# Optimization experiments

Hardware: AMD Instinct MI355X
Metric: run time of the kernel (lower is better)

Reference implementation:

```python
import jax, jax.numpy as jnp
import numpy as np

N_NODES = 100000
N_EDGES = 1600000
IN_DIM = 128
OUT_DIM = 256
EPS = 1e-12


def setup_inputs() -> dict:
    key = jax.random.key(0)
    k1, k2, k3, k4, k5 = jax.random.split(key, 5)
    x = jax.random.normal(k1, (N_NODES, IN_DIM), dtype=jnp.float32)
    edge_index = jax.random.randint(k2, (2, N_EDGES), 0, N_NODES, dtype=jnp.int64)
    edge_weight = jax.random.uniform(k3, (N_EDGES,), dtype=jnp.float32)
    # nn.Linear(in_dim*2, out_dim): weight [out, 2*in], bias [out]
    bound = 1.0 / np.sqrt(2 * IN_DIM)
    W = jax.random.uniform(k4, (OUT_DIM, 2 * IN_DIM), minval=-bound, maxval=bound, dtype=jnp.float32)
    b = jax.random.uniform(k5, (OUT_DIM,), minval=-bound, maxval=bound, dtype=jnp.float32)
    return {"x": x, "edge_index": edge_index, "edge_weight": edge_weight, "W": W, "b": b}


def reference(x, edge_index, edge_weight, W, b):
    src = edge_index[0]
    dst = edge_index[1]
    w = edge_weight.astype(x.dtype)
    # messages: [E, in_dim] = gathered dst features weighted per-edge
    messages = x[dst] * w[:, None]
    agg = jax.ops.segment_sum(messages, src, num_segments=x.shape[0])   # [N, in_dim]
    wsum = jax.ops.segment_sum(w, src, num_segments=x.shape[0])        # [N]
    neigh = agg / jnp.maximum(wsum, EPS)[:, None]
    h = jnp.concatenate([x, neigh], axis=1)                            # [N, 2*in_dim]
    h = h @ W.T + b
    return jax.nn.relu(h)  # dropout is identity in eval / p=0.0
```

## Files before the change

kernel.cpp:

```cpp
#include <hip/hip_runtime.h>
#include <hip/hip_bf16.h>

#define IN_DIM 128
#define OUT_DIM 256
#define KDIM 256
#define EPS 1e-12f
#define CB_NODES 128
#define NB_MAX 1024
#define PART_CHUNK 2048
#define CAP 2560

typedef __attribute__((ext_vector_type(8))) short short8;
typedef __attribute__((ext_vector_type(4))) float f32x4;

static __device__ __forceinline__ unsigned short f2bf(float f) {
  __hip_bfloat16 h = __float2bfloat16(f);
  return *reinterpret_cast<unsigned short*>(&h);
}
static __device__ __forceinline__ unsigned pack2bf(float a, float b) {
  return (unsigned)f2bf(a) | ((unsigned)f2bf(b) << 16);
}
static __device__ __forceinline__ float bf_lo(unsigned v) {
  return __uint_as_float((v & 0xffffu) << 16);
}
static __device__ __forceinline__ float bf_hi(unsigned v) {
  return __uint_as_float(v & 0xffff0000u);
}

__global__ __launch_bounds__(256) void cvt_x(
    const float* __restrict__ x, unsigned short* __restrict__ hb, int N) {
  const int total = N * 32;
  const int stride = gridDim.x * blockDim.x;
  for (int idx = blockIdx.x * blockDim.x + threadIdx.x; idx < total; idx += stride) {
    const int row = idx >> 5;
    const int c4 = (idx & 31) * 4;
    const float4 v = *reinterpret_cast<const float4*>(x + (size_t)row * IN_DIM + c4);
    ushort4 o;
    o.x = f2bf(v.x); o.y = f2bf(v.y); o.z = f2bf(v.z); o.w = f2bf(v.w);
    *reinterpret_cast<ushort4*>(hb + (size_t)row * KDIM + c4) = o;
  }
}

__global__ __launch_bounds__(256) void cvt_w(
    const float* __restrict__ W, unsigned short* __restrict__ Wb) {
  const int base = (blockIdx.x * blockDim.x + threadIdx.x) * 4;
  const float4 v = *reinterpret_cast<const float4*>(W + base);
  ushort4 o;
  o.x = f2bf(v.x); o.y = f2bf(v.y); o.z = f2bf(v.z); o.w = f2bf(v.w);
  *reinterpret_cast<ushort4*>(Wb + base) = o;
}

__global__ __launch_bounds__(256) void chist(
    const int* __restrict__ src, int* __restrict__ cnt, int E, int NB) {
  __shared__ int lcnt[NB_MAX];
  for (int i = threadIdx.x; i < NB; i += 256) lcnt[i] = 0;
  __syncthreads();
  const int stride = gridDim.x * blockDim.x;
  for (int e = blockIdx.x * blockDim.x + threadIdx.x; e < E; e += stride)
    atomicAdd(&lcnt[src[e] >> 7], 1);
  __syncthreads();
  for (int i = threadIdx.x; i < NB; i += 256)
    if (lcnt[i]) atomicAdd(&cnt[i], lcnt[i]);
}

__global__ void cscan(const int* __restrict__ cnt, int* __restrict__ bstart,
                      int* __restrict__ gcursor, int NB) {
  const int lane = threadIdx.x;
  int carry = 0;
  for (int base = 0; base < NB; base += 64) {
    const int i = base + lane;
    const int c = (i < NB) ? cnt[i] : 0;
    int incl = c;
    for (int d = 1; d < 64; d <<= 1) {
      int t = __shfl_up(incl, d, 64);
      if (lane >= d) incl += t;
    }
    const int excl = carry + incl - c;
    if (i < NB) { bstart[i] = excl; gcursor[i] = excl; }
    carry += __shfl(incl, 63, 64);
  }
  if (lane == 0) bstart[NB] = carry;
}

__global__ __launch_bounds__(256) void cpartition(
    const int* __restrict__ src, const int* __restrict__ dst,
    const float* __restrict__ ew,
    int* __restrict__ gcursor, int2* __restrict__ recs, int E, int NB) {
  __shared__ int pos[NB_MAX];
  const int c0 = blockIdx.x * PART_CHUNK;
  const int c1 = min(E, c0 + PART_CHUNK);
  for (int i = threadIdx.x; i < NB; i += 256) pos[i] = 0;
  __syncthreads();
  for (int i = c0 + threadIdx.x; i < c1; i += 256)
    atomicAdd(&pos[src[i] >> 7], 1);
  __syncthreads();
  for (int b = threadIdx.x; b < NB; b += 256) {
    const int c = pos[b];
    pos[b] = c ? atomicAdd(&gcursor[b], c) : 0;
  }
  __syncthreads();
  for (int i = c0 + threadIdx.x; i < c1; i += 256) {
    const int s = src[i];
    const int p = atomicAdd(&pos[s >> 7], 1);
    int2 r;
    r.x = dst[i] | ((s & 127) << 17);
    r.y = __float_as_int(ew[i]);
    recs[p] = r;
  }
}

__global__ __launch_bounds__(512, 8) void cagg_fast(
    unsigned short* __restrict__ hb,
    const int* __restrict__ bstart,
    const int2* __restrict__ recs, int N) {
  __shared__ int2 lrec[CAP];
  __shared__ int lstart[CB_NODES + 1];
  __shared__ int lcur[CB_NODES];
  const int tid = threadIdx.x;
  const int lane = tid & 63;
  const int wv = tid >> 6;
  const int blk = blockIdx.x;
  const int e0 = bstart[blk];
  const int e1 = bstart[blk + 1];
  const int m = e1 - e0;
  if (m > CAP) return;

  if (tid < CB_NODES) lcur[tid] = 0;
  __syncthreads();
  for (int i = tid; i < m; i += 512)
    atomicAdd(&lcur[recs[e0 + i].x >> 17], 1);
  __syncthreads();
  if (wv == 0) {
    int carry = 0;
#pragma unroll
    for (int rr = 0; rr < 2; ++rr) {
      const int idx = rr * 64 + lane;
      const int c = lcur[idx];
      int incl = c;
#pragma unroll
      for (int d = 1; d < 64; d <<= 1) {
        int t = __shfl_up(incl, d, 64);
        if (lane >= d) incl += t;
      }
      lstart[idx] = carry + incl - c;
      carry += __shfl(incl, 63, 64);
    }
    if (lane == 0) lstart[CB_NODES] = carry;
  }
  __syncthreads();
  if (tid < CB_NODES) lcur[tid] = lstart[tid];
  __syncthreads();
  for (int i = tid; i < m; i += 512) {
    const int2 r = recs[e0 + i];
    lrec[atomicAdd(&lcur[r.x >> 17], 1)] = r;
  }
  __syncthreads();

  for (int n = 0; n < 16; ++n) {
    const int rs = lstart[wv * 16 + n];
    const int re = lstart[wv * 16 + n + 1];
    float ax = 0.f, ay = 0.f, ws = 0.f;
    int j = rs;
    for (; j + 8 <= re; j += 8) {
      const int2 r0 = lrec[j + 0];
      const int2 r1 = lrec[j + 1];
      const int2 r2 = lrec[j + 2];
      const int2 r3 = lrec[j + 3];
      const int2 r4 = lrec[j + 4];
      const int2 r5 = lrec[j + 5];
      const int2 r6 = lrec[j + 6];
      const int2 r7 = lrec[j + 7];
      const unsigned v0 = *reinterpret_cast<const unsigned*>(hb + (size_t)(r0.x & 0x1FFFF) * KDIM + lane * 2);
      const unsigned v1 = *reinterpret_cast<const unsigned*>(hb + (size_t)(r1.x & 0x1FFFF) * KDIM + lane * 2);
      const unsigned v2 = *reinterpret_cast<const unsigned*>(hb + (size_t)(r2.x & 0x1FFFF) * KDIM + lane * 2);
      const unsigned v3 = *reinterpret_cast<const unsigned*>(hb + (size_t)(r3.x & 0x1FFFF) * KDIM + lane * 2);
      const unsigned v4 = *reinterpret_cast<const unsigned*>(hb + (size_t)(r4.x & 0x1FFFF) * KDIM + lane * 2);
      const unsigned v5 = *reinterpret_cast<const unsigned*>(hb + (size_t)(r5.x & 0x1FFFF) * KDIM + lane * 2);
      const unsigned v6 = *reinterpret_cast<const unsigned*>(hb + (size_t)(r6.x & 0x1FFFF) * KDIM + lane * 2);
      const unsigned v7 = *reinterpret_cast<const unsigned*>(hb + (size_t)(r7.x & 0x1FFFF) * KDIM + lane * 2);
      const float w0 = __int_as_float(r0.y), w1 = __int_as_float(r1.y);
      const float w2 = __int_as_float(r2.y), w3 = __int_as_float(r3.y);
      const float w4 = __int_as_float(r4.y), w5 = __int_as_float(r5.y);
      const float w6 = __int_as_float(r6.y), w7 = __int_as_float(r7.y);
      ax += bf_lo(v0) * w0 + bf_lo(v1) * w1 + bf_lo(v2) * w2 + bf_lo(v3) * w3
          + bf_lo(v4) * w4 + bf_lo(v5) * w5 + bf_lo(v6) * w6 + bf_lo(v7) * w7;
      ay += bf_hi(v0) * w0 + bf_hi(v1) * w1 + bf_hi(v2) * w2 + bf_hi(v3) * w3
          + bf_hi(v4) * w4 + bf_hi(v5) * w5 + bf_hi(v6) * w6 + bf_hi(v7) * w7;
      ws += w0 + w1 + w2 + w3 + w4 + w5 + w6 + w7;
    }
    for (; j + 2 <= re; j += 2) {
      const int2 r0 = lrec[j + 0];
      const int2 r1 = lrec[j + 1];
      const unsigned v0 = *reinterpret_cast<const unsigned*>(hb + (size_t)(r0.x & 0x1FFFF) * KDIM + lane * 2);
      const unsigned v1 = *reinterpret_cast<const unsigned*>(hb + (size_t)(r1.x & 0x1FFFF) * KDIM + lane * 2);
      const float w0 = __int_as_float(r0.y), w1 = __int_as_float(r1.y);
      ax += bf_lo(v0) * w0 + bf_lo(v1) * w1;
      ay += bf_hi(v0) * w0 + bf_hi(v1) * w1;
      ws += w0 + w1;
    }
    if (j < re) {
      const int2 r = lrec[j];
      const unsigned v = *reinterpret_cast<const unsigned*>(hb + (size_t)(r.x & 0x1FFFF) * KDIM + lane * 2);
      const float w = __int_as_float(r.y);
      ax += bf_lo(v) * w;
      ay += bf_hi(v) * w;
      ws += w;
    }
    const int node = blk * CB_NODES + wv * 16 + n;
    if (node < N) {
      const float mm = fmaxf(ws, EPS);
      *reinterpret_cast<unsigned*>(hb + (size_t)node * KDIM + IN_DIM + lane * 2) =
          pack2bf(ax / mm, ay / mm);
    }
  }
}

__global__ __launch_bounds__(512) void cagg_slow(
    unsigned short* __restrict__ hb,
    const int* __restrict__ bstart,
    const int2* __restrict__ recs, int N) {
  const int blk = blockIdx.x;
  const int e0 = bstart[blk];
  const int e1 = bstart[blk + 1];
  if (e1 - e0 <= CAP) return;

  __shared__ int2 lrec[CAP];
  __shared__ int lstart[CB_NODES + 1];
  __shared__ int lcur[CB_NODES];
  const int tid = threadIdx.x;
  const int lane = tid & 63;
  const int wv = tid >> 6;

  float ax[16], ay[16], ws[16];
#pragma unroll
  for (int n = 0; n < 16; ++n) { ax[n] = 0.f; ay[n] = 0.f; ws[n] = 0.f; }

  for (int base = e0; base < e1; base += CAP) {
    const int m = min(CAP, e1 - base);
    if (tid < CB_NODES) lcur[tid] = 0;
    __syncthreads();
    for (int i = tid; i < m; i += 512)
      atomicAdd(&lcur[recs[base + i].x >> 17], 1);
    __syncthreads();
    if (wv == 0) {
      int carry = 0;
#pragma unroll
      for (int rr = 0; rr < 2; ++rr) {
        const int idx = rr * 64 + lane;
        const int c = lcur[idx];
        int incl = c;
#pragma unroll
        for (int d = 1; d < 64; d <<= 1) {
          int t = __shfl_up(incl, d, 64);
          if (lane >= d) incl += t;
        }
        lstart[idx] = carry + incl - c;
        carry += __shfl(incl, 63, 64);
      }
      if (lane == 0) lstart[CB_NODES] = carry;
    }
    __syncthreads();
    if (tid < CB_NODES) lcur[tid] = lstart[tid];
    __syncthreads();
    for (int i = tid; i < m; i += 512) {
      const int2 r = recs[base + i];
      lrec[atomicAdd(&lcur[r.x >> 17], 1)] = r;
    }
    __syncthreads();
#pragma unroll
    for (int n = 0; n < 16; ++n) {
      const int rs = lstart[wv * 16 + n];
      const int re = lstart[wv * 16 + n + 1];
      for (int j = rs; j < re; ++j) {
        const int2 r = lrec[j];
        const unsigned v = *reinterpret_cast<const unsigned*>(
            hb + (size_t)(r.x & 0x1FFFF) * KDIM + lane * 2);
        const float w = __int_as_float(r.y);
        ax[n] += bf_lo(v) * w;
        ay[n] += bf_hi(v) * w;
        ws[n] += w;
      }
    }
    __syncthreads();
  }

#pragma unroll
  for (int n = 0; n < 16; ++n) {
    const int node = blk * CB_NODES + wv * 16 + n;
    if (node < N) {
      const float mm = fmaxf(ws[n], EPS);
      *reinterpret_cast<unsigned*>(hb + (size_t)node * KDIM + IN_DIM + lane * 2) =
          pack2bf(ax[n] / mm, ay[n] / mm);
    }
  }
}

__global__ __launch_bounds__(512, 2) void sage_gemm_mfma(
    const unsigned short* __restrict__ hb,
    const unsigned short* __restrict__ Wb,
    const float* __restrict__ bias,
    float* __restrict__ out, int N) {
  __shared__ unsigned short Wl[OUT_DIM * KDIM];
  const int tid = threadIdx.x;
  const int lane = tid & 63;
  const int wv = tid >> 6;

  char* wl = reinterpret_cast<char*>(Wl);
  const uint4* wbv = reinterpret_cast<const uint4*>(Wb);
  for (int ch = tid; ch < OUT_DIM * KDIM / 8; ch += 512) {
    const int elem = ch * 8;
    const int j = elem >> 8;
    const int col = elem & 255;
    const uint4 o = wbv[ch];
    const int byte = (j << 9) | ((col * 2) ^ ((j & 7) << 4));
    *reinterpret_cast<uint4*>(wl + byte) = o;
  }

  const int row0 = blockIdx.x * 256 + wv * 32;
  const int kc = (lane >> 4) * 8;
  const unsigned short* arow0 = hb + (size_t)(row0 + (lane & 15)) * KDIM + kc;
  const unsigned short* arow1 = arow0 + 16 * KDIM;
  short8 a0[8], a1[8];
#pragma unroll
  for (int kk = 0; kk < 8; ++kk) {
    a0[kk] = *reinterpret_cast<const short8*>(arow0 + kk * 32);
    a1[kk] = *reinterpret_cast<const short8*>(arow1 + kk * 32);
  }

  __syncthreads();

  f32x4 acc[2][16];
#pragma unroll
  for (int i = 0; i < 2; ++i)
#pragma unroll
    for (int j = 0; j < 16; ++j) acc[i][j] = (f32x4){0.f, 0.f, 0.f, 0.f};

  const int jrow = lane & 15;
  const int kb0 = kc * 2;
#pragma unroll
  for (int kk = 0; kk < 8; ++kk) {
    const int kbyte = kb0 + kk * 64;
#pragma unroll
    for (int ct = 0; ct < 16; ++ct) {
      const int j = ct * 16 + jrow;
      const short8 bf = *reinterpret_cast<const short8*>(
          wl + ((j << 9) | (kbyte ^ ((j & 7) << 4))));
      acc[0][ct] = __builtin_amdgcn_mfma_f32_16x16x32_bf16(a0[kk], bf, acc[0][ct], 0, 0, 0);
      acc[1][ct] = __builtin_amdgcn_mfma_f32_16x16x32_bf16(a1[kk], bf, acc[1][ct], 0, 0, 0);
    }
  }

  const int col = lane & 15;
  const int rquad = (lane >> 4) * 4;
#pragma unroll
  for (int ct = 0; ct < 16; ++ct) {
    const int j = ct * 16 + col;
    const float bj = bias[j];
#pragma unroll
    for (int rt = 0; rt < 2; ++rt) {
      const int rbase = row0 + rt * 16 + rquad;
      const f32x4 a = acc[rt][ct];
#pragma unroll
      for (int r = 0; r < 4; ++r) {
        const int row = rbase + r;
        if (row < N) out[(size_t)row * OUT_DIM + j] = fmaxf(a[r] + bj, 0.f);
      }
    }
  }
}

extern "C" void kernel_launch(void* const* d_in, const int* in_sizes, int n_in,
                              void* d_out, int out_size, void* d_ws, size_t ws_size,
                              hipStream_t stream) {
  const float* x  = (const float*)d_in[0];
  const int*   ei = (const int*)d_in[1];
  const float* ew = (const float*)d_in[2];
  const float* W  = (const float*)d_in[3];
  const float* b  = (const float*)d_in[4];
  float* out = (float*)d_out;

  const int N = in_sizes[0] / IN_DIM;
  const int E = in_sizes[2];
  const int* src = ei;
  const int* dst = ei + E;

  const int gemm_blocks = (N + 255) / 256;
  const int Mpad = gemm_blocks * 256;
  const int NB = (N + CB_NODES - 1) / CB_NODES;

  unsigned short* hb = (unsigned short*)d_ws;
  unsigned short* Wb = hb + (size_t)Mpad * KDIM;
  int2* recs   = (int2*)(Wb + OUT_DIM * KDIM);
  int* cnt     = (int*)(recs + E);
  int* bstart  = cnt + NB_MAX;
  int* gcursor = bstart + NB_MAX + 1;

  hipMemsetAsync(cnt, 0, NB * sizeof(int), stream);

  cvt_x<<<2048, 256, 0, stream>>>(x, hb, N);
  cvt_w<<<OUT_DIM * KDIM / 4 / 256, 256, 0, stream>>>(W, Wb);
  chist<<<512, 256, 0, stream>>>(src, cnt, E, NB);
  cscan<<<1, 64, 0, stream>>>(cnt, bstart, gcursor, NB);
  cpartition<<<(E + PART_CHUNK - 1) / PART_CHUNK, 256, 0, stream>>>(
      src, dst, ew, gcursor, recs, E, NB);
  cagg_fast<<<NB, 512, 0, stream>>>(hb, bstart, recs, N);
  cagg_slow<<<NB, 512, 0, stream>>>(hb, bstart, recs, N);
  sage_gemm_mfma<<<gemm_blocks, 512, 0, stream>>>(hb, Wb, b, out, N);
}
```

Before: 380.6 us.

## Gather neighbor rows with 16-byte loads across four edge groups per wave

The aggregation kernel now splits each wave into four 16-lane groups. Each group handles a different edge and loads 8 bf16 features per lane with uint4 loads, and the partial sums are combined with cross-lane shuffles. Previously every lane loaded 4 bytes per edge. The aim is fewer, wider memory transactions for the random gather. It adds a shuffle reduction per node and a masked tail loop. Separately, the partition kernel caches the src chunk in shared memory so src is not read from global memory twice.

```diff
diff --git a/kernel.cpp b/kernel.cpp
--- a/kernel.cpp
+++ b/kernel.cpp
@@ -87,12 +87,16 @@
     const float* __restrict__ ew,
     int* __restrict__ gcursor, int2* __restrict__ recs, int E, int NB) {
   __shared__ int pos[NB_MAX];
+  __shared__ int ssrc[PART_CHUNK];
   const int c0 = blockIdx.x * PART_CHUNK;
   const int c1 = min(E, c0 + PART_CHUNK);
   for (int i = threadIdx.x; i < NB; i += 256) pos[i] = 0;
   __syncthreads();
-  for (int i = c0 + threadIdx.x; i < c1; i += 256)
-    atomicAdd(&pos[src[i] >> 7], 1);
+  for (int i = c0 + threadIdx.x; i < c1; i += 256) {
+    const int s = src[i];
+    ssrc[i - c0] = s;
+    atomicAdd(&pos[s >> 7], 1);
+  }
   __syncthreads();
   for (int b = threadIdx.x; b < NB; b += 256) {
     const int c = pos[b];
@@ -100,7 +104,7 @@
   }
   __syncthreads();
   for (int i = c0 + threadIdx.x; i < c1; i += 256) {
-    const int s = src[i];
+    const int s = ssrc[i - c0];
     const int p = atomicAdd(&pos[s >> 7], 1);
     int2 r;
     r.x = dst[i] | ((s & 127) << 17);
@@ -156,61 +160,66 @@
   }
   __syncthreads();
 
+  const int g = lane >> 4;
+  const int fl = lane & 15;
   for (int n = 0; n < 16; ++n) {
     const int rs = lstart[wv * 16 + n];
     const int re = lstart[wv * 16 + n + 1];
-    float ax = 0.f, ay = 0.f, ws = 0.f;
-    int j = rs;
-    for (; j + 8 <= re; j += 8) {
-      const int2 r0 = lrec[j + 0];
-      const int2 r1 = lrec[j + 1];
-      const int2 r2 = lrec[j + 2];
-      const int2 r3 = lrec[j + 3];
-      const int2 r4 = lrec[j + 4];
-      const int2 r5 = lrec[j + 5];
-      const int2 r6 = lrec[j + 6];
-      const int2 r7 = lrec[j + 7];
-      const unsigned v0 = *reinterpret_cast<const unsigned*>(hb + (size_t)(r0.x & 0x1FFFF) * KDIM + lane * 2);
-      const unsigned v1 = *reinterpret_cast<const unsigned*>(hb + (size_t)(r1.x & 0x1FFFF) * KDIM + lane * 2);
-      const unsigned v2 = *reinterpret_cast<const unsigned*>(hb + (size_t)(r2.x & 0x1FFFF) * KDIM + lane * 2);
-      const unsigned v3 = *reinterpret_cast<const unsigned*>(hb + (size_t)(r3.x & 0x1FFFF) * KDIM + lane * 2);
-      const unsigned v4 = *reinterpret_cast<const unsigned*>(hb + (size_t)(r4.x & 0x1FFFF) * KDIM + lane * 2);
-      const unsigned v5 = *reinterpret_cast<const unsigned*>(hb + (size_t)(r5.x & 0x1FFFF) * KDIM + lane * 2);
-      const unsigned v6 = *reinterpret_cast<const unsigned*>(hb + (size_t)(r6.x & 0x1FFFF) * KDIM + lane * 2);
-      const unsigned v7 = *reinterpret_cast<const unsigned*>(hb + (size_t)(r7.x & 0x1FFFF) * KDIM + lane * 2);
+    float a0 = 0.f, a1 = 0.f, a2 = 0.f, a3 = 0.f;
+    float a4 = 0.f, a5 = 0.f, a6 = 0.f, a7 = 0.f, ws = 0.f;
+    int j0 = rs;
+    for (; j0 + 16 <= re; j0 += 16) {
+      const int e = j0 + g;
+      const int2 r0 = lrec[e];
+      const int2 r1 = lrec[e + 4];
+      const int2 r2 = lrec[e + 8];
+      const int2 r3 = lrec[e + 12];
+      const uint4 v0 = *reinterpret_cast<const uint4*>(hb + (size_t)(r0.x & 0x1FFFF) * KDIM + fl * 8);
+      const uint4 v1 = *reinterpret_cast<const uint4*>(hb + (size_t)(r1.x & 0x1FFFF) * KDIM + fl * 8);
+      const uint4 v2 = *reinterpret_cast<const uint4*>(hb + (size_t)(r2.x & 0x1FFFF) * KDIM + fl * 8);
+      const uint4 v3 = *reinterpret_cast<const uint4*>(hb + (size_t)(r3.x & 0x1FFFF) * KDIM + fl * 8);
       const float w0 = __int_as_float(r0.y), w1 = __int_as_float(r1.y);
       const float w2 = __int_as_float(r2.y), w3 = __int_as_float(r3.y);
-      const float w4 = __int_as_float(r4.y), w5 = __int_as_float(r5.y);
-      const float w6 = __int_as_float(r6.y), w7 = __int_as_float(r7.y);
-      ax += bf_lo(v0) * w0 + bf_lo(v1) * w1 + bf_lo(v2) * w2 + bf_lo(v3) * w3
-          + bf_lo(v4) * w4 + bf_lo(v5) * w5 + bf_lo(v6) * w6 + bf_lo(v7) * w7;
-      ay += bf_hi(v0) * w0 + bf_hi(v1) * w1 + bf_hi(v2) * w2 + bf_hi(v3) * w3
-          + bf_hi(v4) * w4 + bf_hi(v5) * w5 + bf_hi(v6) * w6 + bf_hi(v7) * w7;
-      ws += w0 + w1 + w2 + w3 + w4 + w5 + w6 + w7;
-    }
-    for (; j + 2 <= re; j += 2) {
-      const int2 r0 = lrec[j + 0];
-      const int2 r1 = lrec[j + 1];
-      const unsigned v0 = *reinterpret_cast<const unsigned*>(hb + (size_t)(r0.x & 0x1FFFF) * KDIM + lane * 2);
-      const unsigned v1 = *reinterpret_cast<const unsigned*>(hb + (size_t)(r1.x & 0x1FFFF) * KDIM + lane * 2);
-      const float w0 = __int_as_float(r0.y), w1 = __int_as_float(r1.y);
-      ax += bf_lo(v0) * w0 + bf_lo(v1) * w1;
-      ay += bf_hi(v0) * w0 + bf_hi(v1) * w1;
-      ws += w0 + w1;
-    }
-    if (j < re) {
-      const int2 r = lrec[j];
-      const unsigned v = *reinterpret_cast<const unsigned*>(hb + (size_t)(r.x & 0x1FFFF) * KDIM + lane * 2);
-      const float w = __int_as_float(r.y);
-      ax += bf_lo(v) * w;
-      ay += bf_hi(v) * w;
+      a0 += bf_lo(v0.x) * w0 + bf_lo(v1.x) * w1 + bf_lo(v2.x) * w2 + bf_lo(v3.x) * w3;
+      a1 += bf_hi(v0.x) * w0 + bf_hi(v1.x) * w1 + bf_hi(v2.x) * w2 + bf_hi(v3.x) * w3;
+      a2 += bf_lo(v0.y) * w0 + bf_lo(v1.y) * w1 + bf_lo(v2.y) * w2 + bf_lo(v3.y) * w3;
+      a3 += bf_hi(v0.y) * w0 + bf_hi(v1.y) * w1 + bf_hi(v2.y) * w2 + bf_hi(v3.y) * w3;
+      a4 += bf_lo(v0.z) * w0 + bf_lo(v1.z) * w1 + bf_lo(v2.z) * w2 + bf_lo(v3.z) * w3;
+      a5 += bf_hi(v0.z) * w0 + bf_hi(v1.z) * w1 + bf_hi(v2.z) * w2 + bf_hi(v3.z) * w3;
+      a6 += bf_lo(v0.w) * w0 + bf_lo(v1.w) * w1 + bf_lo(v2.w) * w2 + bf_lo(v3.w) * w3;
+      a7 += bf_hi(v0.w) * w0 + bf_hi(v1.w) * w1 + bf_hi(v2.w) * w2 + bf_hi(v3.w) * w3;
+      ws += w0 + w1 + w2 + w3;
+    }
+    for (; j0 < re; j0 += 4) {
+      const int e = j0 + g;
+      const bool act = e < re;
+      const int2 r = lrec[act ? e : rs];
+      const float w = act ? __int_as_float(r.y) : 0.f;
+      const uint4 v = *reinterpret_cast<const uint4*>(hb + (size_t)(r.x & 0x1FFFF) * KDIM + fl * 8);
+      a0 += bf_lo(v.x) * w; a1 += bf_hi(v.x) * w;
+      a2 += bf_lo(v.y) * w; a3 += bf_hi(v.y) * w;
+      a4 += bf_lo(v.z) * w; a5 += bf_hi(v.z) * w;
+      a6 += bf_lo(v.w) * w; a7 += bf_hi(v.w) * w;
       ws += w;
     }
+    a0 += __shfl_xor(a0, 16, 64); a0 += __shfl_xor(a0, 32, 64);
+    a1 += __shfl_xor(a1, 16, 64); a1 += __shfl_xor(a1, 32, 64);
+    a2 += __shfl_xor(a2, 16, 64); a2 += __shfl_xor(a2, 32, 64);
+    a3 += __shfl_xor(a3, 16, 64); a3 += __shfl_xor(a3, 32, 64);
+    a4 += __shfl_xor(a4, 16, 64); a4 += __shfl_xor(a4, 32, 64);
+    a5 += __shfl_xor(a5, 16, 64); a5 += __shfl_xor(a5, 32, 64);
+    a6 += __shfl_xor(a6, 16, 64); a6 += __shfl_xor(a6, 32, 64);
+    a7 += __shfl_xor(a7, 16, 64); a7 += __shfl_xor(a7, 32, 64);
+    ws += __shfl_xor(ws, 16, 64); ws += __shfl_xor(ws, 32, 64);
     const int node = blk * CB_NODES + wv * 16 + n;
-    if (node < N) {
-      const float mm = fmaxf(ws, EPS);
-      *reinterpret_cast<unsigned*>(hb + (size_t)node * KDIM + IN_DIM + lane * 2) =
-          pack2bf(ax / mm, ay / mm);
+    if (g == 0 && node < N) {
+      const float inv = 1.0f / fmaxf(ws, EPS);
+      uint4 o;
+      o.x = pack2bf(a0 * inv, a1 * inv);
+      o.y = pack2bf(a2 * inv, a3 * inv);
+      o.z = pack2bf(a4 * inv, a5 * inv);
+      o.w = pack2bf(a6 * inv, a7 * inv);
+      *reinterpret_cast<uint4*>(hb + (size_t)node * KDIM + IN_DIM + fl * 8) = o;
     }
   }
 }
```

After: 382.1 us. No clear change (+0.4%).
